# Optimization experiments

Hardware: AMD Instinct MI355X
Metric: run time of the kernel (lower is better)

The kernel has to match this reference:

```python
import jax, jax.numpy as jnp
import numpy as np

N_NODES = 50000
N_EDGES = 800000
D = 128
N_LAYERS = 3
BN_EPS = 1e-5


def setup_inputs() -> dict:
    key = jax.random.key(0)
    ks = jax.random.split(key, 12)
    x = jax.random.normal(ks[0], (N_NODES, D), dtype=jnp.float32)
    edge_index = jax.random.randint(ks[1], (2, N_EDGES), 0, N_NODES, dtype=jnp.int64)
    edge_attr = jnp.zeros((N_EDGES,), dtype=jnp.int32)  # unused by BaseGIN
    edge_weight = jax.random.uniform(ks[2], (N_EDGES,), dtype=jnp.float32)
    s = 1.0 / np.sqrt(D)
    W1 = jax.random.uniform(ks[3], (N_LAYERS, D, D), minval=-s, maxval=s, dtype=jnp.float32)
    b1 = jax.random.uniform(ks[4], (N_LAYERS, D), minval=-s, maxval=s, dtype=jnp.float32)
    W2 = jax.random.uniform(ks[5], (N_LAYERS, D, D), minval=-s, maxval=s, dtype=jnp.float32)
    b2 = jax.random.uniform(ks[6], (N_LAYERS, D), minval=-s, maxval=s, dtype=jnp.float32)
    eps = jnp.zeros((N_LAYERS,), dtype=jnp.float32)          # GIN epsilon, init 0
    gamma = jnp.ones((N_LAYERS, D), dtype=jnp.float32)       # BN weight
    beta = jnp.zeros((N_LAYERS, D), dtype=jnp.float32)       # BN bias
    return {"x": x, "edge_index": edge_index, "edge_attr": edge_attr,
            "edge_weight": edge_weight, "W1": W1, "b1": b1, "W2": W2,
            "b2": b2, "eps": eps, "gamma": gamma, "beta": beta}


def reference(x, edge_index, edge_attr, edge_weight, W1, b1, W2, b2, eps, gamma, beta):
    del edge_attr  # deleted in BaseGIN.forward
    src, dst = edge_index[0], edge_index[1]
    ew = edge_weight[:, None]  # [E, 1], matches edge_weight[:, None] in torch
    n = x.shape[0]
    for i in range(N_LAYERS):
        # GINConv: propagate = scatter-add of gathered x[src] * edge_weight
        msg = x[src] * ew                                   # [E, D]
        agg = jax.ops.segment_sum(msg, dst, num_segments=n)  # [N, D]
        h = (1.0 + eps[i]) * x + agg
        # MLP: Linear -> ReLU -> Linear
        h = jnp.maximum(h @ W1[i] + b1[i], 0.0) @ W2[i] + b2[i]
        # BatchNorm1d (training-mode batch statistics, biased variance)
        mu = jnp.mean(h, axis=0)
        var = jnp.mean((h - mu) ** 2, axis=0)
        h = gamma[i] * (h - mu) * jax.lax.rsqrt(var + BN_EPS) + beta[i]
        h = jnp.maximum(h, 0.0)  # ReLU (dropout p=0.0 -> identity)
        x = x + h  # residual
    return x
```

## Files before the change

kernel.cpp:

```cpp
#include <hip/hip_runtime.h>

#define NN 50000
#define NE 800000
#define DD 128
#define D4 32
#define NBUCK 196
#define CAP 5120
#define BIN_EDGES 2048

typedef __attribute__((ext_vector_type(8))) short short8;
typedef __attribute__((ext_vector_type(4))) float f32x4;

__device__ __forceinline__ unsigned short f2bf(float f) {
    unsigned u = __float_as_uint(f);
    unsigned r = u + 0x7FFF + ((u >> 16) & 1);
    return (unsigned short)(r >> 16);
}
__device__ __forceinline__ float bf2f(unsigned short s) {
    return __uint_as_float(((unsigned)s) << 16);
}


#define X2B_NB 6250
#define WT_NB 384

__global__ void setup_kernel(const float4* __restrict__ xin, const float* __restrict__ W1,
                             const float* __restrict__ W2, ushort4* __restrict__ xb,
                             unsigned short* __restrict__ Wt, int* __restrict__ bcur) {
    int bid = blockIdx.x;
    int tid = threadIdx.x;
    if (bid < X2B_NB) {
        int i = bid * 256 + tid;
        float4 v = xin[i];
        ushort4 o;
        o.x = f2bf(v.x); o.y = f2bf(v.y); o.z = f2bf(v.z); o.w = f2bf(v.w);
        xb[i] = o;
    } else if (bid < X2B_NB + WT_NB) {
        int i = (bid - X2B_NB) * 256 + tid;
        int m = i >> 14;
        int r = i & 16383;
        int n = r >> 7;
        int k = r & 127;
        const float* Ws = (m < 3) ? (W1 + m * 16384) : (W2 + (m - 3) * 16384);
        Wt[i] = f2bf(Ws[k * 128 + n]);
    } else {
        if (tid < NBUCK) bcur[tid] = tid * CAP;
    }
}


__global__ void __launch_bounds__(256) bin_pass(const int* __restrict__ ei,
                                                const float* __restrict__ ew,
                                                int* __restrict__ bcur,
                                                int2* __restrict__ staging) {
    __shared__ int cnt[256], base[256], cur[256];
    int tid = threadIdx.x;
    int e0 = blockIdx.x * BIN_EDGES;
    int ne = NE - e0; if (ne > BIN_EDGES) ne = BIN_EDGES;
    cnt[tid] = 0;
    cur[tid] = 0;
    __syncthreads();
    int dstv[BIN_EDGES / 256];
    unsigned packv[BIN_EDGES / 256];
#pragma unroll
    for (int j = 0; j < BIN_EDGES / 256; j++) {
        int i = j * 256 + tid;
        dstv[j] = -1;
        if (i < ne) {
            int e = e0 + i;
            int dst = ei[NE + e];
            dstv[j] = dst;
            packv[j] = (((unsigned)ei[e]) << 16) | (unsigned)f2bf(ew[e]);
            atomicAdd(&cnt[dst >> 8], 1);
        }
    }
    __syncthreads();
    if (tid < NBUCK && cnt[tid] > 0) base[tid] = atomicAdd(&bcur[tid], cnt[tid]);
    __syncthreads();
#pragma unroll
    for (int j = 0; j < BIN_EDGES / 256; j++) {
        int dst = dstv[j];
        if (dst >= 0) {
            int b = dst >> 8;
            int p = atomicAdd(&cur[b], 1);
            staging[base[b] + p] = make_int2((int)packv[j], dst & 255);
        }
    }
}

__global__ void scan_buckets(const int* __restrict__ bcur, int* __restrict__ bb2) {
    __shared__ int sh[256];
    int tid = threadIdx.x;
    int c = (tid < NBUCK) ? (bcur[tid] - tid * CAP) : 0;
    sh[tid] = c;
    __syncthreads();
    for (int o = 1; o < 256; o <<= 1) {
        int v = sh[tid];
        int add = (tid >= o) ? sh[tid - o] : 0;
        __syncthreads();
        sh[tid] = v + add;
        __syncthreads();
    }
    if (tid < NBUCK) bb2[tid] = sh[tid] - c;
}

__global__ void __launch_bounds__(256) place_pass(const int2* __restrict__ staging,
                                                  const int* __restrict__ bcur,
                                                  const int* __restrict__ bb2,
                                                  int* __restrict__ rowptr,
                                                  unsigned* __restrict__ srcw) {
    __shared__ int hist[256], off[256], cur[256];
    __shared__ unsigned outb[CAP];
    int b = blockIdx.x;
    int tid = threadIdx.x;
    int sbase = b * CAP;
    int nb = bcur[b] - sbase;
    int bucketBase = bb2[b];
    hist[tid] = 0;
    __syncthreads();
    for (int i = tid; i < nb; i += 256) atomicAdd(&hist[staging[sbase + i].y], 1);
    __syncthreads();
    off[tid] = hist[tid];
    __syncthreads();
    for (int o = 1; o < 256; o <<= 1) {
        int v = off[tid];
        int add = (tid >= o) ? off[tid - o] : 0;
        __syncthreads();
        off[tid] = v + add;
        __syncthreads();
    }
    int excl = off[tid] - hist[tid];
    cur[tid] = excl;
    int node = b * 256 + tid;
    if (node < NN) rowptr[node] = bucketBase + excl;
    if (b == 0 && tid == 0) rowptr[NN] = NE;
    __syncthreads();
    for (int i = tid; i < nb; i += 256) {
        int2 r = staging[sbase + i];
        int p = atomicAdd(&cur[r.y], 1);
        outb[p] = (unsigned)r.x;
    }
    __syncthreads();
    for (int i = tid; i < nb; i += 256) srcw[bucketBase + i] = outb[i];
}


__global__ void __launch_bounds__(256) gather_kernel(
    const unsigned short* __restrict__ xb, const unsigned* __restrict__ srcw,
    const int* __restrict__ rowptr, const float* __restrict__ epsp,
    unsigned short* __restrict__ g, float* __restrict__ stats) {
    if (blockIdx.x == 0) stats[threadIdx.x] = 0.f;
    int node = blockIdx.x * 8 + (threadIdx.x >> 5);
    int lane = threadIdx.x & 31;
    if (node >= NN) return;
    float epsv = 1.0f + *epsp;
    int beg = rowptr[node], end = rowptr[node + 1];
    const ushort4* xb4 = (const ushort4*)xb;
    ushort4 xv = xb4[node * D4 + lane];
    float4 acc = make_float4(bf2f(xv.x) * epsv, bf2f(xv.y) * epsv,
                             bf2f(xv.z) * epsv, bf2f(xv.w) * epsv);
    int i = beg;
    for (; i + 3 < end; i += 4) {
        unsigned sw0 = srcw[i], sw1 = srcw[i + 1], sw2 = srcw[i + 2], sw3 = srcw[i + 3];
        ushort4 r0 = xb4[(sw0 >> 16) * D4 + lane];
        ushort4 r1 = xb4[(sw1 >> 16) * D4 + lane];
        ushort4 r2 = xb4[(sw2 >> 16) * D4 + lane];
        ushort4 r3 = xb4[(sw3 >> 16) * D4 + lane];
        float w0 = bf2f((unsigned short)(sw0 & 0xffff));
        float w1 = bf2f((unsigned short)(sw1 & 0xffff));
        float w2 = bf2f((unsigned short)(sw2 & 0xffff));
        float w3 = bf2f((unsigned short)(sw3 & 0xffff));
        acc.x += bf2f(r0.x) * w0; acc.y += bf2f(r0.y) * w0;
        acc.z += bf2f(r0.z) * w0; acc.w += bf2f(r0.w) * w0;
        acc.x += bf2f(r1.x) * w1; acc.y += bf2f(r1.y) * w1;
        acc.z += bf2f(r1.z) * w1; acc.w += bf2f(r1.w) * w1;
        acc.x += bf2f(r2.x) * w2; acc.y += bf2f(r2.y) * w2;
        acc.z += bf2f(r2.z) * w2; acc.w += bf2f(r2.w) * w2;
        acc.x += bf2f(r3.x) * w3; acc.y += bf2f(r3.y) * w3;
        acc.z += bf2f(r3.z) * w3; acc.w += bf2f(r3.w) * w3;
    }
    for (; i < end; i++) {
        unsigned sw = srcw[i];
        ushort4 r = xb4[(sw >> 16) * D4 + lane];
        float w = bf2f((unsigned short)(sw & 0xffff));
        acc.x += bf2f(r.x) * w; acc.y += bf2f(r.y) * w;
        acc.z += bf2f(r.z) * w; acc.w += bf2f(r.w) * w;
    }
    ushort4 o;
    o.x = f2bf(acc.x); o.y = f2bf(acc.y); o.z = f2bf(acc.z); o.w = f2bf(acc.w);
    ((ushort4*)g)[node * D4 + lane] = o;
}


#define GM 64

__global__ void __launch_bounds__(256) mlp_fused(
    const unsigned short* __restrict__ A,
    const unsigned short* __restrict__ Wt1,
    const unsigned short* __restrict__ Wt2,
    const float* __restrict__ b1, const float* __restrict__ b2,
    unsigned short* __restrict__ outB, float* __restrict__ stats) {
    __shared__ unsigned short As[GM * 128];
    __shared__ unsigned short Ts[GM * 128];

    int tid = threadIdx.x;
    int wave = tid >> 6;
    int lane = tid & 63;
    int q = lane >> 4;
    int ml = lane & 15;
    int r0 = blockIdx.x * GM;

#pragma unroll
    for (int i = 0; i < GM / 16; i++) {
        int idx = i * 256 + tid;
        int row = idx >> 4;
        int c = idx & 15;
        float4 v = make_float4(0.f, 0.f, 0.f, 0.f);
        int grow = r0 + row;
        if (grow < NN) v = *(const float4*)(A + grow * DD + c * 8);
        int cs = c ^ (row & 15);
        *(float4*)(&As[row * DD + cs * 8]) = v;
    }

    short8 Bf1[2][4], Bf2[2][4];
#pragma unroll
    for (int t = 0; t < 2; t++)
#pragma unroll
        for (int ks = 0; ks < 4; ks++) {
            int n = wave * 32 + t * 16 + ml;
            Bf1[t][ks] = *(const short8*)(Wt1 + n * DD + ks * 32 + q * 8);
            Bf2[t][ks] = *(const short8*)(Wt2 + n * DD + ks * 32 + q * 8);
        }
    float bvl1[2] = {b1[wave * 32 + ml], b1[wave * 32 + 16 + ml]};
    float bvl2[2] = {b2[wave * 32 + ml], b2[wave * 32 + 16 + ml]};

    __syncthreads();

    for (int rt = 0; rt < GM / 16; rt++) {
        int arow = rt * 16 + ml;
        short8 Af[4];
#pragma unroll
        for (int ks = 0; ks < 4; ks++) {
            int cs = (ks * 4 + q) ^ (arow & 15);
            Af[ks] = *(const short8*)(&As[arow * DD + cs * 8]);
        }
        f32x4 acc[2] = {{0.f, 0.f, 0.f, 0.f}, {0.f, 0.f, 0.f, 0.f}};
#pragma unroll
        for (int ks = 0; ks < 4; ks++) {
            acc[0] = __builtin_amdgcn_mfma_f32_16x16x32_bf16(Af[ks], Bf1[0][ks], acc[0], 0, 0, 0);
            acc[1] = __builtin_amdgcn_mfma_f32_16x16x32_bf16(Af[ks], Bf1[1][ks], acc[1], 0, 0, 0);
        }
#pragma unroll
        for (int t = 0; t < 2; t++) {
            int col = wave * 32 + t * 16 + ml;
#pragma unroll
            for (int r = 0; r < 4; r++) {
                int lrow = rt * 16 + q * 4 + r;
                unsigned short u = f2bf(fmaxf(acc[t][r] + bvl1[t], 0.f));
                Ts[lrow * DD + ((((col >> 3) ^ (lrow & 15)) << 3) | (col & 7))] = u;
            }
        }
    }
    __syncthreads();

    float s[2] = {0.f, 0.f}, s2[2] = {0.f, 0.f};
    for (int rt = 0; rt < GM / 16; rt++) {
        int arow = rt * 16 + ml;
        short8 Af[4];
#pragma unroll
        for (int ks = 0; ks < 4; ks++) {
            int cs = (ks * 4 + q) ^ (arow & 15);
            Af[ks] = *(const short8*)(&Ts[arow * DD + cs * 8]);
        }
        f32x4 acc[2] = {{0.f, 0.f, 0.f, 0.f}, {0.f, 0.f, 0.f, 0.f}};
#pragma unroll
        for (int ks = 0; ks < 4; ks++) {
            acc[0] = __builtin_amdgcn_mfma_f32_16x16x32_bf16(Af[ks], Bf2[0][ks], acc[0], 0, 0, 0);
            acc[1] = __builtin_amdgcn_mfma_f32_16x16x32_bf16(Af[ks], Bf2[1][ks], acc[1], 0, 0, 0);
        }
#pragma unroll
        for (int t = 0; t < 2; t++) {
            int col = wave * 32 + t * 16 + ml;
#pragma unroll
            for (int r = 0; r < 4; r++) {
                int grow = r0 + rt * 16 + q * 4 + r;
                if (grow < NN) {
                    float v = acc[t][r] + bvl2[t];
                    outB[grow * DD + col] = f2bf(v);
                    s[t] += v;
                    s2[t] += v * v;
                }
            }
        }
    }

#pragma unroll
    for (int t = 0; t < 2; t++) {
        float a = s[t], b = s2[t];
        a += __shfl_xor(a, 16); b += __shfl_xor(b, 16);
        a += __shfl_xor(a, 32); b += __shfl_xor(b, 32);
        if (q == 0) {
            int col = wave * 32 + t * 16 + ml;
            atomicAdd(&stats[col], a);
            atomicAdd(&stats[DD + col], b);
        }
    }
}


__global__ void bn_apply(const unsigned short* __restrict__ hb, const float* __restrict__ stats,
                         const float* __restrict__ gamma, const float* __restrict__ beta,
                         const unsigned short* __restrict__ xbin, ushort4* __restrict__ xbout,
                         float4* __restrict__ xf32) {
    int i = blockIdx.x * blockDim.x + threadIdx.x;
    if (i >= NN * D4) return;
    int c4 = i & 31;
    const float invN = 1.0f / NN;
    float4 s = ((const float4*)stats)[c4];
    float4 s2 = ((const float4*)stats)[D4 + c4];
    float4 mu = make_float4(s.x * invN, s.y * invN, s.z * invN, s.w * invN);
    float4 var = make_float4(s2.x * invN - mu.x * mu.x, s2.y * invN - mu.y * mu.y,
                             s2.z * invN - mu.z * mu.z, s2.w * invN - mu.w * mu.w);
    float4 inv = make_float4(rsqrtf(var.x + 1e-5f), rsqrtf(var.y + 1e-5f),
                             rsqrtf(var.z + 1e-5f), rsqrtf(var.w + 1e-5f));
    float4 g = ((const float4*)gamma)[c4];
    float4 b = ((const float4*)beta)[c4];
    ushort4 hu = ((const ushort4*)hb)[i];
    float4 hv = make_float4(bf2f(hu.x), bf2f(hu.y), bf2f(hu.z), bf2f(hu.w));
    ushort4 xu = ((const ushort4*)xbin)[i];
    float4 xv = make_float4(bf2f(xu.x), bf2f(xu.y), bf2f(xu.z), bf2f(xu.w));
    float4 v = make_float4(fmaxf(g.x * (hv.x - mu.x) * inv.x + b.x, 0.f),
                           fmaxf(g.y * (hv.y - mu.y) * inv.y + b.y, 0.f),
                           fmaxf(g.z * (hv.z - mu.z) * inv.z + b.z, 0.f),
                           fmaxf(g.w * (hv.w - mu.w) * inv.w + b.w, 0.f));
    float4 o = make_float4(xv.x + v.x, xv.y + v.y, xv.z + v.z, xv.w + v.w);
    if (xbout) {
        ushort4 ob;
        ob.x = f2bf(o.x); ob.y = f2bf(o.y); ob.z = f2bf(o.z); ob.w = f2bf(o.w);
        xbout[i] = ob;
    }
    if (xf32) xf32[i] = o;
}


extern "C" void kernel_launch(void* const* d_in, const int* in_sizes, int n_in,
                              void* d_out, int out_size, void* d_ws, size_t ws_size,
                              hipStream_t stream) {
    const float* x_in = (const float*)d_in[0];
    const int* ei = (const int*)d_in[1];
    const float* ew = (const float*)d_in[3];
    const float* W1 = (const float*)d_in[4];
    const float* b1 = (const float*)d_in[5];
    const float* W2 = (const float*)d_in[6];
    const float* b2 = (const float*)d_in[7];
    const float* eps = (const float*)d_in[8];
    const float* gamma = (const float*)d_in[9];
    const float* beta = (const float*)d_in[10];

    float* x = (float*)d_out;

    char* ws = (char*)d_ws;
    unsigned short* g = (unsigned short*)ws;
    unsigned short* hb = (unsigned short*)(ws + 12800000);
    int2* staging = (int2*)(ws + 12800000);
    unsigned short* xb = (unsigned short*)(ws + 25600000);
    float* stats = (float*)(ws + 38400000);
    int* rowptr = (int*)(ws + 38401024);
    unsigned short* Wtall = (unsigned short*)(ws + 38601216);
    unsigned* srcw = (unsigned*)(ws + 38797824);
    int* bcur = (int*)(ws + 41997824);
    int* bb2 = (int*)(ws + 41998848);

    const int n4x = NN * D4;

    setup_kernel<<<X2B_NB + WT_NB + 1, 256, 0, stream>>>(
        (const float4*)x_in, W1, W2, (ushort4*)xb, Wtall, bcur);

    bin_pass<<<(NE + BIN_EDGES - 1) / BIN_EDGES, 256, 0, stream>>>(ei, ew, bcur, staging);
    scan_buckets<<<1, 256, 0, stream>>>(bcur, bb2);
    place_pass<<<NBUCK, 256, 0, stream>>>(staging, bcur, bb2, rowptr, srcw);

    const int gemmGrid = (NN + GM - 1) / GM;

    for (int i = 0; i < 3; i++) {
        const unsigned short* Wt1 = Wtall + i * 16384;
        const unsigned short* Wt2 = Wtall + (3 + i) * 16384;

        gather_kernel<<<(NN + 7) / 8, 256, 0, stream>>>(xb, srcw, rowptr, eps + i, g, stats);

        mlp_fused<<<gemmGrid, 256, 0, stream>>>(g, Wt1, Wt2, b1 + i * DD, b2 + i * DD, hb, stats);

        bn_apply<<<(n4x + 255) / 256, 256, 0, stream>>>(
            hb, stats, gamma + i * DD, beta + i * DD, xb,
            (i < 2) ? (ushort4*)xb : nullptr,
            (i == 2) ? (float4*)x : nullptr);
    }
}
```

Measured before the change: 347.4 us.

## Fuse neighbor gather into MLP kernel and fold bucket scan into place pass

```diff
diff --git a/kernel.cpp b/kernel.cpp
--- a/kernel.cpp
+++ b/kernel.cpp
@@ -26,7 +26,8 @@
 
 __global__ void setup_kernel(const float4* __restrict__ xin, const float* __restrict__ W1,
                              const float* __restrict__ W2, ushort4* __restrict__ xb,
-                             unsigned short* __restrict__ Wt, int* __restrict__ bcur) {
+                             unsigned short* __restrict__ Wt, int* __restrict__ bcur,
+                             float* __restrict__ stats) {
     int bid = blockIdx.x;
     int tid = threadIdx.x;
     if (bid < X2B_NB) {
@@ -45,6 +46,9 @@
         Wt[i] = f2bf(Ws[k * 128 + n]);
     } else {
         if (tid < NBUCK) bcur[tid] = tid * CAP;
+        stats[tid] = 0.f;
+        stats[256 + tid] = 0.f;
+        stats[512 + tid] = 0.f;
     }
 }
 
@@ -88,34 +92,27 @@
     }
 }
 
-__global__ void scan_buckets(const int* __restrict__ bcur, int* __restrict__ bb2) {
-    __shared__ int sh[256];
-    int tid = threadIdx.x;
-    int c = (tid < NBUCK) ? (bcur[tid] - tid * CAP) : 0;
-    sh[tid] = c;
-    __syncthreads();
-    for (int o = 1; o < 256; o <<= 1) {
-        int v = sh[tid];
-        int add = (tid >= o) ? sh[tid - o] : 0;
-        __syncthreads();
-        sh[tid] = v + add;
-        __syncthreads();
-    }
-    if (tid < NBUCK) bb2[tid] = sh[tid] - c;
-}
-
 __global__ void __launch_bounds__(256) place_pass(const int2* __restrict__ staging,
                                                   const int* __restrict__ bcur,
-                                                  const int* __restrict__ bb2,
                                                   int* __restrict__ rowptr,
                                                   unsigned* __restrict__ srcw) {
-    __shared__ int hist[256], off[256], cur[256];
+    __shared__ int hist[256], off[256], cur[256], sb[256];
     __shared__ unsigned outb[CAP];
     int b = blockIdx.x;
     int tid = threadIdx.x;
+    int c0 = (tid < NBUCK) ? (bcur[tid] - tid * CAP) : 0;
+    sb[tid] = c0;
+    __syncthreads();
+    for (int o = 1; o < 256; o <<= 1) {
+        int v = sb[tid];
+        int add = (tid >= o) ? sb[tid - o] : 0;
+        __syncthreads();
+        sb[tid] = v + add;
+        __syncthreads();
+    }
+    int bucketBase = (b == 0) ? 0 : sb[b - 1];
     int sbase = b * CAP;
     int nb = bcur[b] - sbase;
-    int bucketBase = bb2[b];
     hist[tid] = 0;
     __syncthreads();
     for (int i = tid; i < nb; i += 256) atomicAdd(&hist[staging[sbase + i].y], 1);
@@ -145,59 +142,12 @@
 }
 
 
-__global__ void __launch_bounds__(256) gather_kernel(
+#define GM 64
+
+__global__ void __launch_bounds__(256) layer_kernel(
     const unsigned short* __restrict__ xb, const unsigned* __restrict__ srcw,
     const int* __restrict__ rowptr, const float* __restrict__ epsp,
-    unsigned short* __restrict__ g, float* __restrict__ stats) {
-    if (blockIdx.x == 0) stats[threadIdx.x] = 0.f;
-    int node = blockIdx.x * 8 + (threadIdx.x >> 5);
-    int lane = threadIdx.x & 31;
-    if (node >= NN) return;
-    float epsv = 1.0f + *epsp;
-    int beg = rowptr[node], end = rowptr[node + 1];
-    const ushort4* xb4 = (const ushort4*)xb;
-    ushort4 xv = xb4[node * D4 + lane];
-    float4 acc = make_float4(bf2f(xv.x) * epsv, bf2f(xv.y) * epsv,
-                             bf2f(xv.z) * epsv, bf2f(xv.w) * epsv);
-    int i = beg;
-    for (; i + 3 < end; i += 4) {
-        unsigned sw0 = srcw[i], sw1 = srcw[i + 1], sw2 = srcw[i + 2], sw3 = srcw[i + 3];
-        ushort4 r0 = xb4[(sw0 >> 16) * D4 + lane];
-        ushort4 r1 = xb4[(sw1 >> 16) * D4 + lane];
-        ushort4 r2 = xb4[(sw2 >> 16) * D4 + lane];
-        ushort4 r3 = xb4[(sw3 >> 16) * D4 + lane];
-        float w0 = bf2f((unsigned short)(sw0 & 0xffff));
-        float w1 = bf2f((unsigned short)(sw1 & 0xffff));
-        float w2 = bf2f((unsigned short)(sw2 & 0xffff));
-        float w3 = bf2f((unsigned short)(sw3 & 0xffff));
-        acc.x += bf2f(r0.x) * w0; acc.y += bf2f(r0.y) * w0;
-        acc.z += bf2f(r0.z) * w0; acc.w += bf2f(r0.w) * w0;
-        acc.x += bf2f(r1.x) * w1; acc.y += bf2f(r1.y) * w1;
-        acc.z += bf2f(r1.z) * w1; acc.w += bf2f(r1.w) * w1;
-        acc.x += bf2f(r2.x) * w2; acc.y += bf2f(r2.y) * w2;
-        acc.z += bf2f(r2.z) * w2; acc.w += bf2f(r2.w) * w2;
-        acc.x += bf2f(r3.x) * w3; acc.y += bf2f(r3.y) * w3;
-        acc.z += bf2f(r3.z) * w3; acc.w += bf2f(r3.w) * w3;
-    }
-    for (; i < end; i++) {
-        unsigned sw = srcw[i];
-        ushort4 r = xb4[(sw >> 16) * D4 + lane];
-        float w = bf2f((unsigned short)(sw & 0xffff));
-        acc.x += bf2f(r.x) * w; acc.y += bf2f(r.y) * w;
-        acc.z += bf2f(r.z) * w; acc.w += bf2f(r.w) * w;
-    }
-    ushort4 o;
-    o.x = f2bf(acc.x); o.y = f2bf(acc.y); o.z = f2bf(acc.z); o.w = f2bf(acc.w);
-    ((ushort4*)g)[node * D4 + lane] = o;
-}
-
-
-#define GM 64
-
-__global__ void __launch_bounds__(256) mlp_fused(
-    const unsigned short* __restrict__ A,
-    const unsigned short* __restrict__ Wt1,
-    const unsigned short* __restrict__ Wt2,
+    const unsigned short* __restrict__ Wt1, const unsigned short* __restrict__ Wt2,
     const float* __restrict__ b1, const float* __restrict__ b2,
     unsigned short* __restrict__ outB, float* __restrict__ stats) {
     __shared__ unsigned short As[GM * 128];
@@ -210,18 +160,6 @@
     int ml = lane & 15;
     int r0 = blockIdx.x * GM;
 
-#pragma unroll
-    for (int i = 0; i < GM / 16; i++) {
-        int idx = i * 256 + tid;
-        int row = idx >> 4;
-        int c = idx & 15;
-        float4 v = make_float4(0.f, 0.f, 0.f, 0.f);
-        int grow = r0 + row;
-        if (grow < NN) v = *(const float4*)(A + grow * DD + c * 8);
-        int cs = c ^ (row & 15);
-        *(float4*)(&As[row * DD + cs * 8]) = v;
-    }
-
     short8 Bf1[2][4], Bf2[2][4];
 #pragma unroll
     for (int t = 0; t < 2; t++)
@@ -234,6 +172,52 @@
     float bvl1[2] = {b1[wave * 32 + ml], b1[wave * 32 + 16 + ml]};
     float bvl2[2] = {b2[wave * 32 + ml], b2[wave * 32 + 16 + ml]};
 
+    int grp = tid >> 5;
+    int gl = tid & 31;
+    float epsv = 1.0f + *epsp;
+    const ushort4* xb4 = (const ushort4*)xb;
+    for (int j = 0; j < 8; j++) {
+        int row = grp * 8 + j;
+        int node = r0 + row;
+        float4 acc = make_float4(0.f, 0.f, 0.f, 0.f);
+        if (node < NN) {
+            ushort4 xv = xb4[node * D4 + gl];
+            acc = make_float4(bf2f(xv.x) * epsv, bf2f(xv.y) * epsv,
+                              bf2f(xv.z) * epsv, bf2f(xv.w) * epsv);
+            int beg = rowptr[node], end = rowptr[node + 1];
+            int i = beg;
+            for (; i + 3 < end; i += 4) {
+                unsigned sw0 = srcw[i], sw1 = srcw[i + 1], sw2 = srcw[i + 2], sw3 = srcw[i + 3];
+                ushort4 p0 = xb4[(sw0 >> 16) * D4 + gl];
+                ushort4 p1 = xb4[(sw1 >> 16) * D4 + gl];
+                ushort4 p2 = xb4[(sw2 >> 16) * D4 + gl];
+                ushort4 p3 = xb4[(sw3 >> 16) * D4 + gl];
+                float w0 = bf2f((unsigned short)(sw0 & 0xffff));
+                float w1 = bf2f((unsigned short)(sw1 & 0xffff));
+                float w2 = bf2f((unsigned short)(sw2 & 0xffff));
+                float w3 = bf2f((unsigned short)(sw3 & 0xffff));
+                acc.x += bf2f(p0.x) * w0; acc.y += bf2f(p0.y) * w0;
+                acc.z += bf2f(p0.z) * w0; acc.w += bf2f(p0.w) * w0;
+                acc.x += bf2f(p1.x) * w1; acc.y += bf2f(p1.y) * w1;
+                acc.z += bf2f(p1.z) * w1; acc.w += bf2f(p1.w) * w1;
+                acc.x += bf2f(p2.x) * w2; acc.y += bf2f(p2.y) * w2;
+                acc.z += bf2f(p2.z) * w2; acc.w += bf2f(p2.w) * w2;
+                acc.x += bf2f(p3.x) * w3; acc.y += bf2f(p3.y) * w3;
+                acc.z += bf2f(p3.z) * w3; acc.w += bf2f(p3.w) * w3;
+            }
+            for (; i < end; i++) {
+                unsigned sw = srcw[i];
+                ushort4 p = xb4[(sw >> 16) * D4 + gl];
+                float w = bf2f((unsigned short)(sw & 0xffff));
+                acc.x += bf2f(p.x) * w; acc.y += bf2f(p.y) * w;
+                acc.z += bf2f(p.z) * w; acc.w += bf2f(p.w) * w;
+            }
+        }
+        ushort4 o;
+        o.x = f2bf(acc.x); o.y = f2bf(acc.y); o.z = f2bf(acc.z); o.w = f2bf(acc.w);
+        int cs = (gl >> 1) ^ (row & 15);
+        *(ushort4*)(&As[row * DD + cs * 8 + (gl & 1) * 4]) = o;
+    }
     __syncthreads();
 
     for (int rt = 0; rt < GM / 16; rt++) {
@@ -360,38 +344,35 @@
     float* x = (float*)d_out;
 
     char* ws = (char*)d_ws;
-    unsigned short* g = (unsigned short*)ws;
-    unsigned short* hb = (unsigned short*)(ws + 12800000);
-    int2* staging = (int2*)(ws + 12800000);
-    unsigned short* xb = (unsigned short*)(ws + 25600000);
-    float* stats = (float*)(ws + 38400000);
-    int* rowptr = (int*)(ws + 38401024);
-    unsigned short* Wtall = (unsigned short*)(ws + 38601216);
-    unsigned* srcw = (unsigned*)(ws + 38797824);
-    int* bcur = (int*)(ws + 41997824);
-    int* bb2 = (int*)(ws + 41998848);
+    unsigned short* hb = (unsigned short*)ws;
+    int2* staging = (int2*)ws;
+    unsigned short* xb = (unsigned short*)(ws + 12800000);
+    float* stats = (float*)(ws + 25600000);
+    int* rowptr = (int*)(ws + 25603072);
+    unsigned short* Wtall = (unsigned short*)(ws + 25803264);
+    unsigned* srcw = (unsigned*)(ws + 25999872);
+    int* bcur = (int*)(ws + 29199872);
 
     const int n4x = NN * D4;
 
     setup_kernel<<<X2B_NB + WT_NB + 1, 256, 0, stream>>>(
-        (const float4*)x_in, W1, W2, (ushort4*)xb, Wtall, bcur);
+        (const float4*)x_in, W1, W2, (ushort4*)xb, Wtall, bcur, stats);
 
     bin_pass<<<(NE + BIN_EDGES - 1) / BIN_EDGES, 256, 0, stream>>>(ei, ew, bcur, staging);
-    scan_buckets<<<1, 256, 0, stream>>>(bcur, bb2);
-    place_pass<<<NBUCK, 256, 0, stream>>>(staging, bcur, bb2, rowptr, srcw);
+    place_pass<<<NBUCK, 256, 0, stream>>>(staging, bcur, rowptr, srcw);
 
     const int gemmGrid = (NN + GM - 1) / GM;
 
     for (int i = 0; i < 3; i++) {
         const unsigned short* Wt1 = Wtall + i * 16384;
         const unsigned short* Wt2 = Wtall + (3 + i) * 16384;
-
-        gather_kernel<<<(NN + 7) / 8, 256, 0, stream>>>(xb, srcw, rowptr, eps + i, g, stats);
-
-        mlp_fused<<<gemmGrid, 256, 0, stream>>>(g, Wt1, Wt2, b1 + i * DD, b2 + i * DD, hb, stats);
+        float* statsL = stats + i * 256;
+
+        layer_kernel<<<gemmGrid, 256, 0, stream>>>(
+            xb, srcw, rowptr, eps + i, Wt1, Wt2, b1 + i * DD, b2 + i * DD, hb, statsL);
 
         bn_apply<<<(n4x + 255) / 256, 256, 0, stream>>>(
-            hb, stats, gamma + i * DD, beta + i * DD, xb,
+            hb, statsL, gamma + i * DD, beta + i * DD, xb,
             (i < 2) ? (ushort4*)xb : nullptr,
             (i == 2) ? (float4*)x : nullptr);
     }
```

After: 463.6 us. +33.4%, slower.
